# Optimization experiments

Hardware: AMD Instinct MI355X
Metric: run time of the kernel (lower is better)

Reference implementation:

```python
import jax, jax.numpy as jnp
import numpy as np

B, S, F, H = 64, 1024, 128, 512  # batch, seq_len, features, lstm units


def setup_inputs() -> dict:
    key = jax.random.key(0)
    k1, k2, k3 = jax.random.split(key, 3)
    x = jax.random.normal(k1, (B, S, F), dtype=jnp.float32)
    # Keras LSTM params: kernel [F, 4H], recurrent_kernel [H, 4H], bias [4H]
    W = jax.random.normal(k2, (F, 4 * H), dtype=jnp.float32) * (1.0 / np.sqrt(F))
    U = jax.random.normal(k3, (H, 4 * H), dtype=jnp.float32) * (1.0 / np.sqrt(H))
    b = jnp.zeros((4 * H,), dtype=jnp.float32)
    return {"x": x, "W": W, "U": U, "b": b}


def _lstm_relu(x, W, U, b):
    # Precompute input projection for all timesteps: [B,S,4H]
    xW = jnp.einsum("bsf,fg->bsg", x, W) + b
    xW_t = jnp.transpose(xW, (1, 0, 2))  # [S,B,4H] for scan over time
    h0 = jnp.zeros((x.shape[0], H), dtype=x.dtype)
    c0 = jnp.zeros((x.shape[0], H), dtype=x.dtype)

    def step(carry, xw):
        h, c = carry
        z = xw + h @ U  # [B,4H]
        zi, zf, zg, zo = jnp.split(z, 4, axis=-1)  # Keras gate order i,f,c,o
        i = jax.nn.sigmoid(zi)
        f = jax.nn.sigmoid(zf)
        g = jax.nn.relu(zg)          # activation='relu' (candidate)
        o = jax.nn.sigmoid(zo)
        c_new = f * c + i * g
        h_new = o * jax.nn.relu(c_new)  # activation='relu' (output)
        return (h_new, c_new), h_new

    _, hs = jax.lax.scan(step, (h0, c0), xW_t)
    return jnp.transpose(hs, (1, 0, 2))  # [B,S,H]


def reference(x, W, U, b):
    # LSTM(return_sequences=True, activation='relu'); Dropout inactive at inference.
    return _lstm_relu(x, W, U, b)
```

## Files before the change

kernel.cpp:

```cpp
#include <hip/hip_runtime.h>
#include <stdint.h>


#define S_ 1024
#define F_ 128
#define H_ 512
#define G4_ 2048
#define KH 16
#define KDIM 640
#define LDKS 648
#define HB (64 * H_)
#define FLW 32

typedef __attribute__((ext_vector_type(8))) short short8;
typedef __attribute__((ext_vector_type(4))) float f32x4;
typedef unsigned long long ull;

__device__ __forceinline__ unsigned short f2bf(float f) {
  union { float f; unsigned u; } v; v.f = f;
  unsigned u = v.u + 0x7fffu + ((v.u >> 16) & 1u);
  return (unsigned short)(u >> 16);
}

__device__ __forceinline__ short8 pack2(f32x4 a, f32x4 b) {
  short8 r;
#pragma unroll
  for (int i = 0; i < 4; ++i) r[i] = (short)f2bf(a[i]);
#pragma unroll
  for (int i = 0; i < 4; ++i) r[4 + i] = (short)f2bf(b[i]);
  return r;
}

__global__ __launch_bounds__(256, 1) void lstm_pers(
    const float* __restrict__ x, const float* __restrict__ W,
    const float* __restrict__ U, const float* __restrict__ bias,
    float* __restrict__ out, unsigned int* ws_sync, unsigned short* hbuf) {

  __shared__ unsigned short V[64 * LDKS];
  __shared__ f32x4 R[4][4][64];
  __shared__ int meta[2];

  const int tid  = threadIdx.x;
  const int w    = tid >> 6;
  const int lane = tid & 63;
  const int l15  = lane & 15;
  const int l4   = lane >> 4;
  const int koff = l4 * 8;

  if (tid == 0) {
    unsigned int xcc;
    asm volatile("s_getreg_b32 %0, hwreg(20, 0, 4)" : "=s"(xcc));
    xcc &= 7;
    unsigned sv = atomicAdd(ws_sync + xcc * 32, 1u);
    meta[0] = (int)xcc;
    meta[1] = (int)(sv & 31);
  }
  __syncthreads();
  const int xcc  = meta[0];
  const int slot = meta[1];

  unsigned int* gflags = ws_sync + 256 + xcc * (32 * FLW);
  unsigned int* myflag = gflags + slot * FLW + w;
  unsigned int* pollp  = gflags + (8 * w + ((lane & 31) >> 2)) * FLW + (lane & 3);

  const int u0    = slot * 16;
  const int bbase = xcc * 8;

  for (int idx = tid; idx < (64 * KDIM) / 4; idx += 256) {
    const int q4   = idx & 15;
    const int k    = idx >> 4;
    const int gate = q4 & 3;
    const int ul0  = (q4 >> 2) * 4;
    const int col  = gate * H_ + u0 + ul0;
    const float* src = (k < H_) ? (U + (size_t)k * G4_ + col)
                                : (W + (size_t)(k - H_) * G4_ + col);
    const f32x4 v4 = *(const f32x4*)src;
#pragma unroll
    for (int q = 0; q < 4; ++q) {
      const int ul = ul0 + q;
      const int cc = (ul >> 2) * 16 + (ul & 3) * 4 + gate;
      V[cc * LDKS + k] = f2bf(v4[q]);
    }
  }

  float bias_r[4];
#pragma unroll
  for (int g = 0; g < 4; ++g) bias_r[g] = bias[g * H_ + u0 + w * 4 + l4];

  __syncthreads();

  const int brow = bbase + (l15 & 7);
  const float* xrow = x + (size_t)brow * S_ * F_ + koff + w * 32;
  const unsigned short* hrow0 = hbuf + (size_t)brow * H_ + koff;
  const int myunit = u0 + w * 4 + l4;

  float cst = 0.f;

  f32x4 xa = *(const f32x4*)(xrow);
  f32x4 xb = *(const f32x4*)(xrow + 4);

  for (int t = 0; t < S_; ++t) {
    f32x4 acc[4];
#pragma unroll
    for (int tl = 0; tl < 4; ++tl) { acc[tl][0]=0.f; acc[tl][1]=0.f; acc[tl][2]=0.f; acc[tl][3]=0.f; }
    {
      const short8 bx = pack2(xa, xb);
      const int k0 = (KH + w) * 32 + koff;
#pragma unroll
      for (int tl = 0; tl < 4; ++tl) {
        const short8 a = *(const short8*)&V[(tl * 16 + l15) * LDKS + k0];
        acc[tl] = __builtin_amdgcn_mfma_f32_16x16x32_bf16(a, bx, acc[tl], 0, 0, 0);
      }
    }

    {
      const int tn = (t + 1 < S_) ? t + 1 : t;
      const float* xt = xrow + (size_t)tn * F_;
      xa = *(const f32x4*)(xt);
      xb = *(const f32x4*)(xt + 4);
    }

    if (t > 0) {
      const unsigned tgt = (unsigned)t;
      while (true) {
        const unsigned v = __hip_atomic_load(pollp, __ATOMIC_RELAXED, __HIP_MEMORY_SCOPE_AGENT);
        if (__all((int)(v >= tgt))) break;
      }

      const unsigned short* hr = hrow0 + (size_t)(t & 1) * HB;
      short8 bh[4];
#pragma unroll
      for (int i = 0; i < 4; ++i) {
        union { ull u[2]; short8 s; } bb;
        const ull* hq = (const ull*)(hr + (4 * w + i) * 32);
        bb.u[0] = __hip_atomic_load(hq,     __ATOMIC_RELAXED, __HIP_MEMORY_SCOPE_AGENT);
        bb.u[1] = __hip_atomic_load(hq + 1, __ATOMIC_RELAXED, __HIP_MEMORY_SCOPE_AGENT);
        bh[i] = bb.s;
      }
#pragma unroll
      for (int i = 0; i < 4; ++i) {
        const int k0 = (4 * w + i) * 32 + koff;
#pragma unroll
        for (int tl = 0; tl < 4; ++tl) {
          const short8 a = *(const short8*)&V[(tl * 16 + l15) * LDKS + k0];
          acc[tl] = __builtin_amdgcn_mfma_f32_16x16x32_bf16(a, bh[i], acc[tl], 0, 0, 0);
        }
      }
    }

#pragma unroll
    for (int tl = 0; tl < 4; ++tl) R[w][tl][lane] = acc[tl];
    __syncthreads();

    f32x4 z;
    {
      const f32x4 r0 = R[0][w][lane], r1 = R[1][w][lane],
                  r2 = R[2][w][lane], r3 = R[3][w][lane];
#pragma unroll
      for (int g = 0; g < 4; ++g)
        z[g] = bias_r[g] + r0[g] + r1[g] + r2[g] + r3[g];
    }

    const float ig = 1.f / (1.f + __expf(-z[0]));
    const float fg = 1.f / (1.f + __expf(-z[1]));
    const float gg = fmaxf(z[2], 0.f);
    const float og = 1.f / (1.f + __expf(-z[3]));
    const float cn = fg * cst + ig * gg;
    cst = cn;
    const float hv = og * fmaxf(cn, 0.f);

    if (l15 < 8)
      hbuf[(size_t)((t + 1) & 1) * HB + (size_t)brow * H_ + myunit] = f2bf(hv);
    asm volatile("s_waitcnt vmcnt(0)" ::: "memory");

    if (lane == 0)
      __hip_atomic_store(myflag, (unsigned)(t + 1),
                         __ATOMIC_RELAXED, __HIP_MEMORY_SCOPE_AGENT);

    if (l15 < 8)
      out[((size_t)brow * S_ + t) * H_ + myunit] = hv;
  }
}

extern "C" void kernel_launch(void* const* d_in, const int* in_sizes, int n_in,
                              void* d_out, int out_size, void* d_ws, size_t ws_size,
                              hipStream_t stream) {
  const float* x = (const float*)d_in[0];
  const float* W = (const float*)d_in[1];
  const float* U = (const float*)d_in[2];
  const float* b = (const float*)d_in[3];
  float* out = (float*)d_out;

  unsigned int*   ws_sync = (unsigned int*)d_ws;
  unsigned short* hbuf    = (unsigned short*)((char*)d_ws + 65536);

  hipMemsetAsync(d_ws, 0, 65536, stream);

  lstm_pers<<<dim3(256), dim3(256), 0, stream>>>(x, W, U, b, out, ws_sync, hbuf);
}
```

Before: 2.472 ms.

## Replace flag-based step sync with sign-bit tagged hidden-state polling

```diff
diff --git a/kernel.cpp b/kernel.cpp
--- a/kernel.cpp
+++ b/kernel.cpp
@@ -10,7 +10,8 @@
 #define KDIM 640
 #define LDKS 648
 #define HB (64 * H_)
-#define FLW 32
+#define SMASK8 0x8000800080008000ull
+#define VMASK8 0x7FFF7FFF7FFF7FFFull
 
 typedef __attribute__((ext_vector_type(8))) short short8;
 typedef __attribute__((ext_vector_type(4))) float f32x4;
@@ -59,10 +60,6 @@
   const int xcc  = meta[0];
   const int slot = meta[1];
 
-  unsigned int* gflags = ws_sync + 256 + xcc * (32 * FLW);
-  unsigned int* myflag = gflags + slot * FLW + w;
-  unsigned int* pollp  = gflags + (8 * w + ((lane & 31) >> 2)) * FLW + (lane & 3);
-
   const int u0    = slot * 16;
   const int bbase = xcc * 8;
 
@@ -121,22 +118,32 @@
     }
 
     if (t > 0) {
-      const unsigned tgt = (unsigned)t;
+      const ull expm = (((((unsigned)(t - 1)) >> 1) & 1u) ^ 1u) ? SMASK8 : 0ull;
+      const unsigned short* hr = hrow0 + (size_t)(t & 1) * HB;
+      const ull* q0 = (const ull*)(hr + (4 * w + 0) * 32);
+      const ull* q1 = (const ull*)(hr + (4 * w + 1) * 32);
+      const ull* q2 = (const ull*)(hr + (4 * w + 2) * 32);
+      const ull* q3 = (const ull*)(hr + (4 * w + 3) * 32);
+      ull d0, d1, d2, d3, d4, d5, d6, d7;
       while (true) {
-        const unsigned v = __hip_atomic_load(pollp, __ATOMIC_RELAXED, __HIP_MEMORY_SCOPE_AGENT);
-        if (__all((int)(v >= tgt))) break;
+        d0 = __hip_atomic_load(q0,     __ATOMIC_RELAXED, __HIP_MEMORY_SCOPE_AGENT);
+        d1 = __hip_atomic_load(q0 + 1, __ATOMIC_RELAXED, __HIP_MEMORY_SCOPE_AGENT);
+        d2 = __hip_atomic_load(q1,     __ATOMIC_RELAXED, __HIP_MEMORY_SCOPE_AGENT);
+        d3 = __hip_atomic_load(q1 + 1, __ATOMIC_RELAXED, __HIP_MEMORY_SCOPE_AGENT);
+        d4 = __hip_atomic_load(q2,     __ATOMIC_RELAXED, __HIP_MEMORY_SCOPE_AGENT);
+        d5 = __hip_atomic_load(q2 + 1, __ATOMIC_RELAXED, __HIP_MEMORY_SCOPE_AGENT);
+        d6 = __hip_atomic_load(q3,     __ATOMIC_RELAXED, __HIP_MEMORY_SCOPE_AGENT);
+        d7 = __hip_atomic_load(q3 + 1, __ATOMIC_RELAXED, __HIP_MEMORY_SCOPE_AGENT);
+        const ull bad = (d0 ^ expm) | (d1 ^ expm) | (d2 ^ expm) | (d3 ^ expm) |
+                        (d4 ^ expm) | (d5 ^ expm) | (d6 ^ expm) | (d7 ^ expm);
+        if (__all((int)((bad & SMASK8) == 0ull))) break;
       }
-
-      const unsigned short* hr = hrow0 + (size_t)(t & 1) * HB;
-      short8 bh[4];
-#pragma unroll
-      for (int i = 0; i < 4; ++i) {
-        union { ull u[2]; short8 s; } bb;
-        const ull* hq = (const ull*)(hr + (4 * w + i) * 32);
-        bb.u[0] = __hip_atomic_load(hq,     __ATOMIC_RELAXED, __HIP_MEMORY_SCOPE_AGENT);
-        bb.u[1] = __hip_atomic_load(hq + 1, __ATOMIC_RELAXED, __HIP_MEMORY_SCOPE_AGENT);
-        bh[i] = bb.s;
-      }
+      union { ull u[2]; short8 s; } b0, b1, b2, b3;
+      b0.u[0] = d0 & VMASK8; b0.u[1] = d1 & VMASK8;
+      b1.u[0] = d2 & VMASK8; b1.u[1] = d3 & VMASK8;
+      b2.u[0] = d4 & VMASK8; b2.u[1] = d5 & VMASK8;
+      b3.u[0] = d6 & VMASK8; b3.u[1] = d7 & VMASK8;
+      const short8 bh[4] = {b0.s, b1.s, b2.s, b3.s};
 #pragma unroll
       for (int i = 0; i < 4; ++i) {
         const int k0 = (4 * w + i) * 32 + koff;
@@ -169,13 +176,18 @@
     cst = cn;
     const float hv = og * fmaxf(cn, 0.f);
 
-    if (l15 < 8)
-      hbuf[(size_t)((t + 1) & 1) * HB + (size_t)brow * H_ + myunit] = f2bf(hv);
-    asm volatile("s_waitcnt vmcnt(0)" ::: "memory");
-
-    if (lane == 0)
-      __hip_atomic_store(myflag, (unsigned)(t + 1),
-                         __ATOMIC_RELAXED, __HIP_MEMORY_SCOPE_AGENT);
+    const unsigned hb0 = (unsigned)f2bf(hv);
+    const unsigned hb1 = (unsigned)__shfl((int)hb0, (lane & 7) + 16);
+    const unsigned hb2 = (unsigned)__shfl((int)hb0, (lane & 7) + 32);
+    const unsigned hb3 = (unsigned)__shfl((int)hb0, (lane & 7) + 48);
+    const ull tagw = ((((unsigned)t >> 1) & 1u) ^ 1u) ? SMASK8 : 0ull;
+    const ull wrd = (ull)(hb0 & 0xFFFFu) | ((ull)(hb1 & 0xFFFFu) << 16) |
+                    ((ull)(hb2 & 0xFFFFu) << 32) | ((ull)(hb3 & 0xFFFFu) << 48) | tagw;
+    if (lane < 8) {
+      ull* dst = (ull*)(hbuf + (size_t)((t + 1) & 1) * HB +
+                        (size_t)(bbase + lane) * H_ + u0 + w * 4);
+      __hip_atomic_store(dst, wrd, __ATOMIC_RELAXED, __HIP_MEMORY_SCOPE_AGENT);
+    }
 
     if (l15 < 8)
       out[((size_t)brow * S_ + t) * H_ + myunit] = hv;
@@ -192,9 +204,9 @@
   float* out = (float*)d_out;
 
   unsigned int*   ws_sync = (unsigned int*)d_ws;
-  unsigned short* hbuf    = (unsigned short*)((char*)d_ws + 65536);
-
-  hipMemsetAsync(d_ws, 0, 65536, stream);
+  unsigned short* hbuf    = (unsigned short*)((char*)d_ws + 1024);
+
+  hipMemsetAsync(d_ws, 0, 1024 + 2 * HB * sizeof(unsigned short), stream);
 
   lstm_pers<<<dim3(256), dim3(256), 0, stream>>>(x, W, U, b, out, ws_sync, hbuf);
 }
```

Result: no change. 2.454 ms (median of 2 runs) (-0.7%).
